# Kernel optimization log

Measured on AMD Instinct MI355X. Metric: run time of the kernel, lower is better.

The kernel has to match this reference:

```python
import jax, jax.numpy as jnp
import numpy as np

B, T, S, D = 64, 512, 512, 256


def setup_inputs() -> dict:
    key = jax.random.key(0)
    ks = jax.random.split(key, 8)
    s = 1.0 / np.sqrt(D)  # pytorch LSTM init scale
    return {
        "decoder_embeds": jax.random.normal(ks[0], (B, T, D), jnp.float32),
        "h0": jax.random.normal(ks[1], (1, B, D), jnp.float32),
        "c0": jax.random.normal(ks[2], (1, B, D), jnp.float32),
        "encoder_output": jax.random.normal(ks[3], (B, S, D), jnp.float32),
        "W_ih": jax.random.uniform(ks[4], (4 * D, D), jnp.float32, -s, s),
        "W_hh": jax.random.uniform(ks[5], (4 * D, D), jnp.float32, -s, s),
        "b_ih": jax.random.uniform(ks[6], (4 * D,), jnp.float32, -s, s),
        "b_hh": jax.random.uniform(ks[7], (4 * D,), jnp.float32, -s, s),
    }


def _lstm_outputs(decoder_embeds, h0, c0, W_ih, W_hh, b_ih, b_hh):
    # Faithful to source: step 0 input is decoder_embeds[:,0]; afterwards the
    # previous LSTM OUTPUT is fed back (decoder_embeds[:,1:] are unused).
    d = decoder_embeds.shape[-1]
    bias = b_ih + b_hh  # [4D]

    def step(carry, _):
        x, h, c = carry  # each [B, D]
        gates = x @ W_ih.T + h @ W_hh.T + bias  # [B, 4D]
        i, f, g, o = jnp.split(gates, 4, axis=-1)  # pytorch gate order i,f,g,o
        c_new = jax.nn.sigmoid(f) * c + jax.nn.sigmoid(i) * jnp.tanh(g)
        h_new = jax.nn.sigmoid(o) * jnp.tanh(c_new)
        return (h_new, h_new, c_new), h_new

    init = (decoder_embeds[:, 0, :], h0[0], c0[0])
    _, H = jax.lax.scan(step, init, None, length=decoder_embeds.shape[1])
    return jnp.transpose(H, (1, 0, 2))  # [B, T, D]


def reference(decoder_embeds, h0, c0, encoder_output, W_ih, W_hh, b_ih, b_hh):
    H = _lstm_outputs(decoder_embeds, h0, c0, W_ih, W_hh, b_ih, b_hh)  # [B,T,D]
    # use_attention=True: per-step bmm attention; h_t only depends on the scan,
    # so attention is computed vectorized over T (same math).
    scores = jnp.einsum("btd,bsd->bts", H, encoder_output)  # [B,T,S]
    attn = jax.nn.softmax(scores, axis=-1)
    ctx = jnp.einsum("bts,bsd->btd", attn, encoder_output)  # [B,T,D]
    return jnp.concatenate([H, ctx], axis=-1)  # [B,T,2D]
```

## Files before the change

### kernel.cpp

```cpp
#include <hip/hip_runtime.h>
#include <cstdint>
#include <cstddef>

#define B_  64
#define T_  512
#define S_  512
#define D_  256

#define GROUPS 16
#define BPG    16

typedef __attribute__((ext_vector_type(4))) float f32x4;
typedef __attribute__((ext_vector_type(8))) short bf16x8;

union UBF { bf16x8 v; uint32_t u[4]; };
union USH { bf16x8 v; ushort s[8]; };

__device__ __forceinline__ ushort f2bf(float f) {
    union { float f; uint32_t u; } v; v.f = f;
    uint32_t r = v.u + 0x7FFFu + ((v.u >> 16) & 1u);
    return (ushort)(r >> 16);
}
__device__ __forceinline__ float bf2f(ushort h) {
    union { uint32_t u; float f; } v; v.u = ((uint32_t)h) << 16; return v.f;
}
__device__ __forceinline__ uint4 ldx4u_cg(const uint32_t* p) {
    uint4 r;
    asm volatile("global_load_dwordx4 %0, %1, off sc0 sc1\n\ts_waitcnt vmcnt(0)"
                 : "=v"(r) : "v"(p) : "memory");
    return r;
}
__device__ __forceinline__ void st_cg_u32(uint32_t* p, uint32_t v) {
    asm volatile("global_store_dword %0, %1, off sc0 sc1" :: "v"(p), "v"(v) : "memory");
}

__global__ __launch_bounds__(256) void ws_init(uint32_t* __restrict__ hbuf) {
    int i = blockIdx.x * 256 + threadIdx.x;
    if (i < 2 * 16384)
        __hip_atomic_store(hbuf + i, 0xFFFFFFFFu, __ATOMIC_RELAXED, __HIP_MEMORY_SCOPE_AGENT);
}


__global__ __launch_bounds__(256, 1) void lstm_persistent(
    const float* __restrict__ de,  const float* __restrict__ h0,
    const float* __restrict__ c0,
    const float* __restrict__ Wih, const float* __restrict__ Whh,
    const float* __restrict__ bih, const float* __restrict__ bhh,
    float* __restrict__ out, uint32_t* __restrict__ hbuf)
{
    __shared__ uint32_t hlds[4 * 264];
    __shared__ float    glds[256];
    __shared__ float    t0buf[2][4][256];

    const int tid = threadIdx.x;
    const int grp = blockIdx.x >> 4;
    const int jb  = blockIdx.x & 15;

    const int w  = tid >> 6;
    const int l  = tid & 63;
    const int lr = l & 15;
    const int lg = l >> 4;

    const int cb  = tid & 3;
    const int cd  = tid >> 2;
    const int bx  = grp * 4 + cb;
    const int dxc = jb * 16 + cd;

    float c_reg = 0.f;
    float bsum0 = 0.f, bsum1 = 0.f, bsum2 = 0.f, bsum3 = 0.f;
    if (tid < 64) {
        c_reg = c0[(size_t)bx * 256 + dxc];
        bsum0 = bih[          jb * 16 + cd] + bhh[          jb * 16 + cd];
        bsum1 = bih[256 +     jb * 16 + cd] + bhh[256 +     jb * 16 + cd];
        bsum2 = bih[512 +     jb * 16 + cd] + bhh[512 +     jb * 16 + cd];
        bsum3 = bih[768 +     jb * 16 + cd] + bhh[768 +     jb * 16 + cd];
    }

    bf16x8 Ahi[8], Alo[8];

    #pragma unroll
    for (int m = 0; m < 8; ++m) {
        int idx = m * 256 + tid;
        int arr = idx >> 10, bl = (idx >> 8) & 3, k = idx & 255;
        t0buf[arr][bl][k] = arr ? h0[(size_t)(grp * 4 + bl) * 256 + k]
                                : de[(size_t)(grp * 4 + bl) * T_ * D_ + k];
    }
    __syncthreads();
    {
        int r = tid >> 2, bq = tid & 3;
        int gr = (r >> 4) * 256 + jb * 16 + (r & 15);
        const float4* wi4 = (const float4*)(Wih + (size_t)gr * 256);
        const float4* wh4 = (const float4*)(Whh + (size_t)gr * 256);
        const float4* e4  = (const float4*)(&t0buf[0][bq][0]);
        const float4* h4  = (const float4*)(&t0buf[1][bq][0]);
        float a0 = 0.f, a1 = 0.f, a2 = 0.f, a3 = 0.f;
        #pragma unroll 8
        for (int k4 = 0; k4 < 64; ++k4) {
            float4 x = wi4[k4], y = e4[k4];
            a0 += x.x*y.x; a1 += x.y*y.y; a2 += x.z*y.z; a3 += x.w*y.w;
            x = wh4[k4]; y = h4[k4];
            a0 += x.x*y.x; a1 += x.y*y.y; a2 += x.z*y.z; a3 += x.w*y.w;
        }
        glds[(r >> 4) * 64 + (r & 15) * 4 + bq] = (a0 + a1) + (a2 + a3);
    }

    for (int t = 0; t < T_; ++t) {
        if (t > 0) {
            const uint32_t expc = (uint32_t)(((t - 1) >> 1) % 3);
            const uint32_t* hp = hbuf + ((t - 1) & 1) * 16384 + grp * 1024 + tid * 4;
            uint4 v = ldx4u_cg(hp);
            while (((v.x & 3u) != expc) | ((v.y & 3u) != expc) |
                   ((v.z & 3u) != expc) | ((v.w & 3u) != expc))
                v = ldx4u_cg(hp);
            *(uint4*)(hlds + (tid >> 6) * 264 + (tid & 63) * 4) = v;
            __syncthreads();

            f32x4 acc = (f32x4){0.f, 0.f, 0.f, 0.f};
            const uint32_t* hrow = hlds + (lr & 3) * 264 + lg * 8;
            #pragma unroll
            for (int kt = 0; kt < 8; ++kt) {
                uint4 q0 = *(const uint4*)(hrow + kt * 32);
                uint4 q1 = *(const uint4*)(hrow + kt * 32 + 4);
                UBF bh_, bl_;
                bh_.u[0] = (q0.x >> 16) | (q0.y & 0xFFFF0000u);
                bh_.u[1] = (q0.z >> 16) | (q0.w & 0xFFFF0000u);
                bh_.u[2] = (q1.x >> 16) | (q1.y & 0xFFFF0000u);
                bh_.u[3] = (q1.z >> 16) | (q1.w & 0xFFFF0000u);
                bl_.u[0] = (q0.x & 0xFFFCu) | ((q0.y & 0xFFFCu) << 16);
                bl_.u[1] = (q0.z & 0xFFFCu) | ((q0.w & 0xFFFCu) << 16);
                bl_.u[2] = (q1.x & 0xFFFCu) | ((q1.y & 0xFFFCu) << 16);
                bl_.u[3] = (q1.z & 0xFFFCu) | ((q1.w & 0xFFFCu) << 16);
                acc = __builtin_amdgcn_mfma_f32_16x16x32_bf16(Ahi[kt], bh_.v, acc, 0, 0, 0);
                acc = __builtin_amdgcn_mfma_f32_16x16x32_bf16(Alo[kt], bh_.v, acc, 0, 0, 0);
                acc = __builtin_amdgcn_mfma_f32_16x16x32_bf16(Ahi[kt], bl_.v, acc, 0, 0, 0);
            }
            if (lr < 4) {
                glds[w * 64 + (lg * 4 + 0) * 4 + lr] = acc[0];
                glds[w * 64 + (lg * 4 + 1) * 4 + lr] = acc[1];
                glds[w * 64 + (lg * 4 + 2) * 4 + lr] = acc[2];
                glds[w * 64 + (lg * 4 + 3) * 4 + lr] = acc[3];
            }
        }
        __syncthreads();

        if (tid < 64) {
            float gi = glds[      cd * 4 + cb] + bsum0;
            float gf = glds[ 64 + cd * 4 + cb] + bsum1;
            float gg = glds[128 + cd * 4 + cb] + bsum2;
            float go = glds[192 + cd * 4 + cb] + bsum3;
            float si = 1.f / (1.f + __expf(-gi));
            float sf = 1.f / (1.f + __expf(-gf));
            float so = 1.f / (1.f + __expf(-go));
            float tg = 1.f - 2.f / (1.f + __expf(2.f * gg));
            c_reg = sf * c_reg + si * tg;
            float tc = 1.f - 2.f / (1.f + __expf(2.f * c_reg));
            float hn = so * tc;
            out[((size_t)bx * T_ + t) * 512 + dxc] = hn;
            if (t < T_ - 1) {
                uint32_t hi = (uint32_t)f2bf(hn);
                float lof   = hn - bf2f((ushort)hi);
                uint32_t lo = (uint32_t)f2bf(lof);
                uint32_t pk = (hi << 16) | (lo & 0xFFFCu) | (uint32_t)((t >> 1) % 3);
                st_cg_u32(hbuf + (t & 1) * 16384 + grp * 1024 + cb * 256 + dxc, pk);
            }
        }

        if (t == 0) {
            int gr = w * 256 + jb * 16 + lr;
            const float4* wi4 = (const float4*)(Wih + (size_t)gr * 256);
            const float4* wh4 = (const float4*)(Whh + (size_t)gr * 256);
            #pragma unroll
            for (int kt = 0; kt < 8; ++kt) {
                float4 p  = wi4[kt * 8 + lg * 2], q  = wi4[kt * 8 + lg * 2 + 1];
                float4 r4 = wh4[kt * 8 + lg * 2], s4 = wh4[kt * 8 + lg * 2 + 1];
                float f[8] = {p.x + r4.x, p.y + r4.y, p.z + r4.z, p.w + r4.w,
                              q.x + s4.x, q.y + s4.y, q.z + s4.z, q.w + s4.w};
                USH hi, lo;
                #pragma unroll
                for (int j = 0; j < 8; ++j) {
                    ushort h = f2bf(f[j]);
                    hi.s[j] = h;
                    lo.s[j] = f2bf(f[j] - bf2f(h));
                }
                Ahi[kt] = hi.v; Alo[kt] = lo.v;
            }
        }
    }
}


__global__ __launch_bounds__(256, 2) void attn_kernel(
    const float* __restrict__ E, float* __restrict__ out)
{
    __shared__ alignas(16) ushort Ech [32 * 264];
    __shared__ alignas(16) ushort EchT[256 * 40];
    __shared__ alignas(16) ushort Phi[4][16 * 40];
    __shared__ alignas(16) ushort Plo[4][16 * 40];

    const int id  = blockIdx.x;
    const int xcd = id & 7, rr = id >> 3;
    const int tt  = rr & 7,  bh = rr >> 3;
    const int b   = bh * 8 + xcd;
    const int t0  = tt * 64;

    const int tid = threadIdx.x;
    const int w   = tid >> 6;
    const int l   = tid & 63;
    const int lr  = l & 15;
    const int lg  = l >> 4;

    bf16x8 Ahi[8], Alo[8];
    {
        const float* Hrow = out + ((size_t)b * T_ + (t0 + w * 16 + lr)) * 512;
        #pragma unroll
        for (int kt = 0; kt < 8; ++kt) {
            float4 x0 = *(const float4*)(Hrow + kt * 32 + lg * 8);
            float4 x1 = *(const float4*)(Hrow + kt * 32 + lg * 8 + 4);
            float f[8] = {x0.x, x0.y, x0.z, x0.w, x1.x, x1.y, x1.z, x1.w};
            USH hi, lo;
            #pragma unroll
            for (int j = 0; j < 8; ++j) {
                ushort h = f2bf(f[j]);
                hi.s[j] = h;
                lo.s[j] = f2bf(f[j] - bf2f(h));
            }
            Ahi[kt] = hi.v; Alo[kt] = lo.v;
        }
    }

    f32x4 ctx[16];
    #pragma unroll
    for (int i = 0; i < 16; ++i) ctx[i] = (f32x4){0.f, 0.f, 0.f, 0.f};
    float mrow[4] = {-1e30f, -1e30f, -1e30f, -1e30f};
    float srow[4] = {0.f, 0.f, 0.f, 0.f};

    const float* Eb = E + (size_t)b * S_ * 256;

    for (int c = 0; c < 16; ++c) {
        #pragma unroll
        for (int m = 0; m < 8; ++m) {
            int idx = m * 256 + tid;
            int sr = idx >> 6, k4 = idx & 63;
            float4 e = *(const float4*)(Eb + (size_t)(c * 32 + sr) * 256 + 4 * k4);
            ushort4 u;
            u.x = f2bf(e.x); u.y = f2bf(e.y); u.z = f2bf(e.z); u.w = f2bf(e.w);
            *(ushort4*)(&Ech[sr * 264 + 4 * k4]) = u;
        }
        __syncthreads();

        f32x4 sacc0 = (f32x4){0.f,0.f,0.f,0.f};
        f32x4 sacc1 = (f32x4){0.f,0.f,0.f,0.f};
        #pragma unroll
        for (int kt = 0; kt < 8; ++kt) {
            bf16x8 Bf0 = *(const bf16x8*)(&Ech[(0 * 16 + lr) * 264 + kt * 32 + lg * 8]);
            bf16x8 Bf1 = *(const bf16x8*)(&Ech[(1 * 16 + lr) * 264 + kt * 32 + lg * 8]);
            sacc0 = __builtin_amdgcn_mfma_f32_16x16x32_bf16(Ahi[kt], Bf0, sacc0, 0, 0, 0);
            sacc0 = __builtin_amdgcn_mfma_f32_16x16x32_bf16(Alo[kt], Bf0, sacc0, 0, 0, 0);
            sacc1 = __builtin_amdgcn_mfma_f32_16x16x32_bf16(Ahi[kt], Bf1, sacc1, 0, 0, 0);
            sacc1 = __builtin_amdgcn_mfma_f32_16x16x32_bf16(Alo[kt], Bf1, sacc1, 0, 0, 0);
        }

        #pragma unroll
        for (int m = 0; m < 8; ++m) {
            int idx = m * 256 + tid;
            int s = idx & 31, kq = idx >> 5;
            ushort4 v = *(const ushort4*)(&Ech[s * 264 + 4 * kq]);
            EchT[(4 * kq + 0) * 40 + s] = v.x;
            EchT[(4 * kq + 1) * 40 + s] = v.y;
            EchT[(4 * kq + 2) * 40 + s] = v.z;
            EchT[(4 * kq + 3) * 40 + s] = v.w;
        }

        float cmax[4], p0[4], p1[4], csum[4], mnew[4], scale[4];
        #pragma unroll
        for (int g = 0; g < 4; ++g) cmax[g] = fmaxf(sacc0[g], sacc1[g]);
        #pragma unroll
        for (int d = 1; d < 16; d <<= 1) {
            #pragma unroll
            for (int g = 0; g < 4; ++g) cmax[g] = fmaxf(cmax[g], __shfl_xor(cmax[g], d));
        }
        #pragma unroll
        for (int g = 0; g < 4; ++g) {
            mnew[g]  = fmaxf(mrow[g], cmax[g]);
            scale[g] = __expf(mrow[g] - mnew[g]);
            p0[g] = __expf(sacc0[g] - mnew[g]);
            p1[g] = __expf(sacc1[g] - mnew[g]);
            csum[g] = p0[g] + p1[g];
        }
        #pragma unroll
        for (int d = 1; d < 16; d <<= 1) {
            #pragma unroll
            for (int g = 0; g < 4; ++g) csum[g] += __shfl_xor(csum[g], d);
        }
        #pragma unroll
        for (int g = 0; g < 4; ++g) {
            srow[g] = srow[g] * scale[g] + csum[g];
            mrow[g] = mnew[g];
        }
        #pragma unroll
        for (int i = 0; i < 16; ++i) {
            ctx[i][0] *= scale[0]; ctx[i][1] *= scale[1];
            ctx[i][2] *= scale[2]; ctx[i][3] *= scale[3];
        }
        #pragma unroll
        for (int g = 0; g < 4; ++g) {
            int rrw = (lg * 4 + g) * 40;
            ushort h0v = f2bf(p0[g]);
            Phi[w][rrw + lr]      = h0v;
            Plo[w][rrw + lr]      = f2bf(p0[g] - bf2f(h0v));
            ushort h1v = f2bf(p1[g]);
            Phi[w][rrw + 16 + lr] = h1v;
            Plo[w][rrw + 16 + lr] = f2bf(p1[g] - bf2f(h1v));
        }
        __syncthreads();

        {
            bf16x8 Ap = *(const bf16x8*)(&Phi[w][lr * 40 + lg * 8]);
            bf16x8 Aq = *(const bf16x8*)(&Plo[w][lr * 40 + lg * 8]);
            #pragma unroll
            for (int dt = 0; dt < 16; ++dt) {
                bf16x8 Bf = *(const bf16x8*)(&EchT[(dt * 16 + lr) * 40 + lg * 8]);
                ctx[dt] = __builtin_amdgcn_mfma_f32_16x16x32_bf16(Ap, Bf, ctx[dt], 0, 0, 0);
                ctx[dt] = __builtin_amdgcn_mfma_f32_16x16x32_bf16(Aq, Bf, ctx[dt], 0, 0, 0);
            }
        }
        __syncthreads();
    }

    float inv[4];
    #pragma unroll
    for (int g = 0; g < 4; ++g) inv[g] = 1.f / srow[g];
    #pragma unroll
    for (int dt = 0; dt < 16; ++dt) {
        #pragma unroll
        for (int g = 0; g < 4; ++g) {
            out[((size_t)b * T_ + (t0 + w * 16 + lg * 4 + g)) * 512 + 256 + dt * 16 + lr] =
                ctx[dt][g] * inv[g];
        }
    }
}


extern "C" void kernel_launch(void* const* d_in, const int* in_sizes, int n_in,
                              void* d_out, int out_size, void* d_ws, size_t ws_size,
                              hipStream_t stream)
{
    const float* de  = (const float*)d_in[0];
    const float* h0  = (const float*)d_in[1];
    const float* c0  = (const float*)d_in[2];
    const float* E   = (const float*)d_in[3];
    const float* Wih = (const float*)d_in[4];
    const float* Whh = (const float*)d_in[5];
    const float* bih = (const float*)d_in[6];
    const float* bhh = (const float*)d_in[7];
    float* out  = (float*)d_out;
    uint32_t* hbuf = (uint32_t*)d_ws;

    ws_init<<<128, 256, 0, stream>>>(hbuf);

    void* args[] = {(void*)&de, (void*)&h0, (void*)&c0, (void*)&Wih, (void*)&Whh,
                    (void*)&bih, (void*)&bhh, (void*)&out, (void*)&hbuf};
    hipLaunchCooperativeKernel((const void*)lstm_persistent,
                               dim3(GROUPS * BPG), dim3(256), args, 0, stream);

    attn_kernel<<<dim3(512), 256, 0, stream>>>(E, out);
}
```

Measured before the change: 1.187 ms.

## Drop low-order h split in recurrent MFMA and use full-step tag word

The hidden state exchanged between blocks is now only the bf16 high part, and the low 16 bits carry the full step index as a readiness tag instead of a mod-3 counter. This removes the Ahi*h_lo MFMA and the split-h packing work, cuts the inner loop to two independent accumulators (hi and lo weights) that can overlap, and packs with a byte-permute. The h store is moved before the output store to shorten the cross-block critical path, and the LDS row padding changes. The cost is lower precision for h in the recurrence (bf16 instead of roughly split-bf16), which can accumulate error over 512 steps.

```diff
diff --git a/kernel.cpp b/kernel.cpp
--- a/kernel.cpp
+++ b/kernel.cpp
@@ -32,6 +32,13 @@
 }
 __device__ __forceinline__ void st_cg_u32(uint32_t* p, uint32_t v) {
     asm volatile("global_store_dword %0, %1, off sc0 sc1" :: "v"(p), "v"(v) : "memory");
+}
+__device__ __forceinline__ uint32_t hi2(uint32_t a, uint32_t b) {
+#if __has_builtin(__builtin_amdgcn_perm)
+    return __builtin_amdgcn_perm(b, a, 0x07060302u);
+#else
+    return (a >> 16) | (b & 0xFFFF0000u);
+#endif
 }
 
 __global__ __launch_bounds__(256) void ws_init(uint32_t* __restrict__ hbuf) {
@@ -48,7 +55,7 @@
     const float* __restrict__ bih, const float* __restrict__ bhh,
     float* __restrict__ out, uint32_t* __restrict__ hbuf)
 {
-    __shared__ uint32_t hlds[4 * 264];
+    __shared__ uint32_t hlds[4 * 260];
     __shared__ float    glds[256];
     __shared__ float    t0buf[2][4][256];
 
@@ -70,10 +77,10 @@
     float bsum0 = 0.f, bsum1 = 0.f, bsum2 = 0.f, bsum3 = 0.f;
     if (tid < 64) {
         c_reg = c0[(size_t)bx * 256 + dxc];
-        bsum0 = bih[          jb * 16 + cd] + bhh[          jb * 16 + cd];
-        bsum1 = bih[256 +     jb * 16 + cd] + bhh[256 +     jb * 16 + cd];
-        bsum2 = bih[512 +     jb * 16 + cd] + bhh[512 +     jb * 16 + cd];
-        bsum3 = bih[768 +     jb * 16 + cd] + bhh[768 +     jb * 16 + cd];
+        bsum0 = bih[      jb * 16 + cd] + bhh[      jb * 16 + cd];
+        bsum1 = bih[256 + jb * 16 + cd] + bhh[256 + jb * 16 + cd];
+        bsum2 = bih[512 + jb * 16 + cd] + bhh[512 + jb * 16 + cd];
+        bsum3 = bih[768 + jb * 16 + cd] + bhh[768 + jb * 16 + cd];
     }
 
     bf16x8 Ahi[8], Alo[8];
@@ -106,34 +113,30 @@
 
     for (int t = 0; t < T_; ++t) {
         if (t > 0) {
-            const uint32_t expc = (uint32_t)(((t - 1) >> 1) % 3);
+            const uint32_t expc = (uint32_t)(t - 1);
             const uint32_t* hp = hbuf + ((t - 1) & 1) * 16384 + grp * 1024 + tid * 4;
             uint4 v = ldx4u_cg(hp);
-            while (((v.x & 3u) != expc) | ((v.y & 3u) != expc) |
-                   ((v.z & 3u) != expc) | ((v.w & 3u) != expc))
+            while ((((v.x ^ expc) | (v.y ^ expc) | (v.z ^ expc) | (v.w ^ expc)) & 0xFFFFu) != 0u)
                 v = ldx4u_cg(hp);
-            *(uint4*)(hlds + (tid >> 6) * 264 + (tid & 63) * 4) = v;
+            *(uint4*)(hlds + (tid >> 6) * 260 + (tid & 63) * 4) = v;
             __syncthreads();
 
-            f32x4 acc = (f32x4){0.f, 0.f, 0.f, 0.f};
-            const uint32_t* hrow = hlds + (lr & 3) * 264 + lg * 8;
+            f32x4 acch = (f32x4){0.f, 0.f, 0.f, 0.f};
+            f32x4 accl = (f32x4){0.f, 0.f, 0.f, 0.f};
+            const uint32_t* hrow = hlds + (lr & 3) * 260 + lg * 8;
             #pragma unroll
             for (int kt = 0; kt < 8; ++kt) {
                 uint4 q0 = *(const uint4*)(hrow + kt * 32);
                 uint4 q1 = *(const uint4*)(hrow + kt * 32 + 4);
-                UBF bh_, bl_;
-                bh_.u[0] = (q0.x >> 16) | (q0.y & 0xFFFF0000u);
-                bh_.u[1] = (q0.z >> 16) | (q0.w & 0xFFFF0000u);
-                bh_.u[2] = (q1.x >> 16) | (q1.y & 0xFFFF0000u);
-                bh_.u[3] = (q1.z >> 16) | (q1.w & 0xFFFF0000u);
-                bl_.u[0] = (q0.x & 0xFFFCu) | ((q0.y & 0xFFFCu) << 16);
-                bl_.u[1] = (q0.z & 0xFFFCu) | ((q0.w & 0xFFFCu) << 16);
-                bl_.u[2] = (q1.x & 0xFFFCu) | ((q1.y & 0xFFFCu) << 16);
-                bl_.u[3] = (q1.z & 0xFFFCu) | ((q1.w & 0xFFFCu) << 16);
-                acc = __builtin_amdgcn_mfma_f32_16x16x32_bf16(Ahi[kt], bh_.v, acc, 0, 0, 0);
-                acc = __builtin_amdgcn_mfma_f32_16x16x32_bf16(Alo[kt], bh_.v, acc, 0, 0, 0);
-                acc = __builtin_amdgcn_mfma_f32_16x16x32_bf16(Ahi[kt], bl_.v, acc, 0, 0, 0);
-            }
+                UBF bb;
+                bb.u[0] = hi2(q0.x, q0.y);
+                bb.u[1] = hi2(q0.z, q0.w);
+                bb.u[2] = hi2(q1.x, q1.y);
+                bb.u[3] = hi2(q1.z, q1.w);
+                acch = __builtin_amdgcn_mfma_f32_16x16x32_bf16(Ahi[kt], bb.v, acch, 0, 0, 0);
+                accl = __builtin_amdgcn_mfma_f32_16x16x32_bf16(Alo[kt], bb.v, accl, 0, 0, 0);
+            }
+            f32x4 acc = acch + accl;
             if (lr < 4) {
                 glds[w * 64 + (lg * 4 + 0) * 4 + lr] = acc[0];
                 glds[w * 64 + (lg * 4 + 1) * 4 + lr] = acc[1];
@@ -155,14 +158,11 @@
             c_reg = sf * c_reg + si * tg;
             float tc = 1.f - 2.f / (1.f + __expf(2.f * c_reg));
             float hn = so * tc;
+            if (t < T_ - 1) {
+                uint32_t pk = ((uint32_t)f2bf(hn) << 16) | (uint32_t)t;
+                st_cg_u32(hbuf + (t & 1) * 16384 + grp * 1024 + cb * 256 + dxc, pk);
+            }
             out[((size_t)bx * T_ + t) * 512 + dxc] = hn;
-            if (t < T_ - 1) {
-                uint32_t hi = (uint32_t)f2bf(hn);
-                float lof   = hn - bf2f((ushort)hi);
-                uint32_t lo = (uint32_t)f2bf(lof);
-                uint32_t pk = (hi << 16) | (lo & 0xFFFCu) | (uint32_t)((t >> 1) % 3);
-                st_cg_u32(hbuf + (t & 1) * 16384 + grp * 1024 + cb * 256 + dxc, pk);
-            }
         }
 
         if (t == 0) {
```

Result: faster. 1.019 ms, median of 2 (-14.1%).
